# Optimization experiments

Measured on AMD Instinct MI355X. Metric: run time of the kernel, lower is better.

The kernel has to match this reference:

```python
import jax, jax.numpy as jnp
import numpy as np
from jax import lax

HIDDEN_MAX_ABS = 1000.0

def _run_layer(x_seq, W_ih, b_ih, w_hh, w_uh, b_uh, h0):
    # x_seq: [T,B,I]; W_ih: [H,I]; w_hh,w_uh,b_ih: [H]; b_uh: scalar; h0: [H]
    w_hh = jnp.clip(w_hh, -HIDDEN_MAX_ABS, HIDDEN_MAX_ABS)  # check_bounds (min_abs=0 is falsy)
    B = x_seq.shape[1]
    Hn = w_hh.shape[0]
    # hoist input projection out of the recurrence
    pre = jnp.einsum('tbi,hi->tbh', x_seq, W_ih) + b_ih  # [T,B,H]
    init = (jnp.broadcast_to(h0, (B, Hn)),
            jnp.ones((B, Hn), x_seq.dtype),
            jnp.zeros((B, Hn), x_seq.dtype))
    def step(carry, pre_t):
        hx, up_prev, cum_prev = carry
        new_hx = jax.nn.relu(pre_t + w_hh * hx)
        tilde = jax.nn.sigmoid(new_hx * w_uh + b_uh)
        cum = cum_prev + jnp.minimum(up_prev, 1.0 - cum_prev)
        # straight-through round (BinaryLayer)
        g = cum + lax.stop_gradient(jnp.round(cum) - cum)
        new_h = g * new_hx + (1.0 - g) * hx
        new_up = g * tilde + (1.0 - g) * up_prev
        new_cum = (1.0 - g) * cum
        return (new_h, new_up, new_cum), (new_h, g)
    _, (outs, gates) = lax.scan(step, init, pre)
    return outs, gates  # each [T,B,H]


def setup_inputs() -> dict:
    key = jax.random.key(0)
    ks = jax.random.split(key, 5)
    T, B, I, H, L = 512, 64, 256, 512, 2
    x = jax.random.normal(ks[0], (T, B, I), dtype=jnp.float32)
    h0 = jax.random.normal(ks[1], (L, H), dtype=jnp.float32)
    W_ih0 = 0.01 * jax.random.normal(ks[2], (H, I), dtype=jnp.float32)
    W_ih1 = 0.01 * jax.random.normal(ks[3], (H, H), dtype=jnp.float32)
    b_ih = jnp.zeros((L, H), jnp.float32)
    w_hh = jnp.ones((L, H), jnp.float32)
    w_uh = jax.random.normal(ks[4], (L, H), dtype=jnp.float32) * float(np.sqrt(2.0 / (1 + H)))
    b_uh = jnp.zeros((L,), jnp.float32)
    return {"x": x, "h0": h0, "W_ih0": W_ih0, "W_ih1": W_ih1,
            "b_ih": b_ih, "w_hh": w_hh, "w_uh": w_uh, "b_uh": b_uh}


def reference(x, h0, W_ih0, W_ih1, b_ih, w_hh, w_uh, b_uh):
    o0, g0 = _run_layer(x, W_ih0, b_ih[0], w_hh[0], w_uh[0], b_uh[0], h0[0])
    o1, g1 = _run_layer(o0, W_ih1, b_ih[1], w_hh[1], w_uh[1], b_uh[1], h0[1])
    # torch stacks layer outputs then .squeeze(); with L=2 no dim is squeezed
    x_out = jnp.stack([o0, o1], 0)      # [L,T,B,H]
    gates = jnp.stack([g0, g1], 0)      # [L,T,B,H]
    return x_out, gates
```

## Files before the change

kernel.cpp:

```cpp
#include <hip/hip_runtime.h>
#include <math.h>

#define TT 512
#define BB 64
#define II 256
#define HH 512
#define BH (BB*HH)
#define TBH ((size_t)TT*BH)
#define MM (TT*BB)

typedef float f32x4 __attribute__((ext_vector_type(4)));
typedef _Float16 f16x8 __attribute__((ext_vector_type(8)));
typedef unsigned short u16;

__device__ __forceinline__ void gload16(const void* g, void* l) {
    __builtin_amdgcn_global_load_lds(
        (const __attribute__((address_space(1))) unsigned int*)g,
        (__attribute__((address_space(3))) unsigned int*)l, 16, 0, 0);
}

__global__ __launch_bounds__(256)
void pack_w2(const float* __restrict__ W0, const float* __restrict__ W1,
             _Float16* __restrict__ P0, _Float16* __restrict__ P1,
             int nf0, int nf1)
{
    const int i = blockIdx.x * 256 + threadIdx.x;
    const float* src; _Float16* dst;
    if (i < nf0) { src = W0 + (size_t)i * 8;  dst = P0 + (size_t)i * 8; }
    else         { const int j = i - nf0; if (j >= nf1) return;
                   src = W1 + (size_t)j * 8;  dst = P1 + (size_t)j * 8; }
    f16x8 h8;
#pragma unroll
    for (int j = 0; j < 8; ++j) h8[j] = (_Float16)src[j];
    *(f16x8*)dst = h8;
}

template<typename OutT>
__global__ __launch_bounds__(256, 4)
void gemm_f32a(const float* __restrict__ A, const _Float16* __restrict__ Bp,
               const float* __restrict__ bias, OutT* __restrict__ C,
               int M, int N, int K)
{
    const int K8 = K >> 3;
    __shared__ _Float16 As[128][40];

    const int tid  = threadIdx.x;
    const int lane = tid & 63;
    const int wid  = tid >> 6;
    const int wr   = wid >> 1, wc = wid & 1;

    const int nbn = N >> 7;
    const int nt  = (M >> 7) * nbn;
    const int per = nt >> 3;
    const int logical = (blockIdx.x & 7) * per + (blockIdx.x >> 3);
    const int bm = logical / nbn;
    const int bn = logical % nbn;
    const int row0 = bm * 128;
    const int col0 = bn * 128;

    const int s_row = tid >> 1;
    const int s_kh  = (tid & 1) * 16;
    const float* Ap = A + (size_t)(row0 + s_row) * K + s_kh;

    const int fr  = lane & 15;
    const int q   = lane >> 4;
    const int ko8 = q * 8;

    f32x4 acc[4][4];
#pragma unroll
    for (int m = 0; m < 4; ++m)
#pragma unroll
        for (int n = 0; n < 4; ++n)
#pragma unroll
            for (int r = 0; r < 4; ++r) acc[m][n][r] = 0.f;

    const _Float16* bbase[4];
#pragma unroll
    for (int n = 0; n < 4; ++n) {
        const int col = col0 + wc * 64 + n * 16 + fr;
        bbase[n] = Bp + ((size_t)col * K8 + q) * 8;
    }

    f32x4 a_ld[4];
#pragma unroll
    for (int qq = 0; qq < 4; ++qq) a_ld[qq] = *(const f32x4*)(Ap + qq * 4);

    const int nkt = K >> 5;
    for (int kt = 0; kt < nkt; ++kt) {
        __syncthreads();
#pragma unroll
        for (int half = 0; half < 2; ++half) {
            f16x8 h8;
#pragma unroll
            for (int j = 0; j < 8; ++j)
                h8[j] = (_Float16)a_ld[half * 2 + (j >> 2)][j & 3];
            *(f16x8*)&As[s_row][s_kh + half * 8] = h8;
        }
        __syncthreads();

        f16x8 bfr[4];
#pragma unroll
        for (int n = 0; n < 4; ++n)
            bfr[n] = *(const f16x8*)(bbase[n] + (size_t)kt * 32);

        if (kt + 1 < nkt) {
            const float* apn = Ap + (size_t)(kt + 1) * 32;
#pragma unroll
            for (int qq = 0; qq < 4; ++qq) a_ld[qq] = *(const f32x4*)(apn + qq * 4);
        }

#pragma unroll
        for (int m = 0; m < 4; ++m) {
            const int row = wr * 64 + m * 16 + fr;
            f16x8 af = *(const f16x8*)&As[row][ko8];
#pragma unroll
            for (int n = 0; n < 4; ++n)
                acc[m][n] = __builtin_amdgcn_mfma_f32_16x16x32_f16(af, bfr[n], acc[m][n], 0, 0, 0);
        }
    }

#pragma unroll
    for (int n = 0; n < 4; ++n) {
        const int gc = col0 + wc * 64 + n * 16 + fr;
        const float bj = bias[gc];
#pragma unroll
        for (int m = 0; m < 4; ++m) {
            const int gr0 = row0 + wr * 64 + m * 16 + q * 4;
#pragma unroll
            for (int r = 0; r < 4; ++r)
                C[(size_t)(gr0 + r) * N + gc] = (OutT)(acc[m][n][r] + bj);
        }
    }
}

template<typename OutT>
__global__ __launch_bounds__(256, 3)
void gemm_f16a(const _Float16* __restrict__ A, const _Float16* __restrict__ Bp,
               const float* __restrict__ bias, OutT* __restrict__ C,
               int M, int N, int K)
{
    const int K8 = K >> 3;
    __shared__ _Float16 As[128 * 32];

    const int tid  = threadIdx.x;
    const int lane = tid & 63;
    const int wid  = tid >> 6;
    const int wr   = wid >> 1, wc = wid & 1;

    const int nbn = N >> 7;
    const int nt  = (M >> 7) * nbn;
    const int per = nt >> 3;
    const int logical = (blockIdx.x & 7) * per + (blockIdx.x >> 3);
    const int bm = logical / nbn;
    const int bn = logical % nbn;
    const int row0 = bm * 128;
    const int col0 = bn * 128;

    const int a_row = lane >> 2;
    const int a_kk  = (lane & 3) * 8;

    const int fr  = lane & 15;
    const int q   = lane >> 4;
    const int ko8 = q * 8;

    f32x4 acc[4][4];
#pragma unroll
    for (int m = 0; m < 4; ++m)
#pragma unroll
        for (int n = 0; n < 4; ++n)
#pragma unroll
            for (int r = 0; r < 4; ++r) acc[m][n][r] = 0.f;

    const _Float16* bbase[4];
#pragma unroll
    for (int n = 0; n < 4; ++n) {
        const int col = col0 + wc * 64 + n * 16 + fr;
        bbase[n] = Bp + ((size_t)col * K8 + q) * 8;
    }

    f16x8 bfr[4], bnf[4];
#pragma unroll
    for (int n = 0; n < 4; ++n) bfr[n] = *(const f16x8*)(bbase[n]);

    const int nkt = K >> 5;
    for (int kt = 0; kt < nkt; ++kt) {
        const int k0 = kt * 32;
        __syncthreads();
#pragma unroll
        for (int i = 0; i < 2; ++i) {
            const int chunk = wid * 2 + i;
            const size_t ga = (size_t)(row0 + chunk * 16 + a_row) * K + k0 + a_kk;
            gload16(A + ga, (char*)&As[0] + chunk * 1024 + (lane & 3) * 16
                               + (size_t)(a_row) * 0);
        }
        __syncthreads();

        if (kt + 1 < nkt) {
#pragma unroll
            for (int n = 0; n < 4; ++n)
                bnf[n] = *(const f16x8*)(bbase[n] + (size_t)(kt + 1) * 32);
        }

#pragma unroll
        for (int m = 0; m < 4; ++m) {
            const int row = wr * 64 + m * 16 + fr;
            f16x8 af = *(const f16x8*)&As[row * 32 + ko8];
#pragma unroll
            for (int n = 0; n < 4; ++n)
                acc[m][n] = __builtin_amdgcn_mfma_f32_16x16x32_f16(af, bfr[n], acc[m][n], 0, 0, 0);
        }
#pragma unroll
        for (int n = 0; n < 4; ++n) bfr[n] = bnf[n];
    }

#pragma unroll
    for (int n = 0; n < 4; ++n) {
        const int gc = col0 + wc * 64 + n * 16 + fr;
        const float bj = bias[gc];
#pragma unroll
        for (int m = 0; m < 4; ++m) {
            const int gr0 = row0 + wr * 64 + m * 16 + q * 4;
#pragma unroll
            for (int r = 0; r < 4; ++r)
                C[(size_t)(gr0 + r) * N + gc] = (OutT)(acc[m][n][r] + bj);
        }
    }
}

template<typename PreT, bool EMITF16, bool NTX, bool NTG>
__global__ __launch_bounds__(64)
void skip_indrnn_rec(const PreT* __restrict__ pre, const float* __restrict__ h0,
                     const float* __restrict__ w_hh, const float* __restrict__ w_uh,
                     const float* __restrict__ b_uh, int layer,
                     float* __restrict__ xo, float* __restrict__ go,
                     _Float16* __restrict__ xo16)
{
    const int idx = blockIdx.x * 64 + threadIdx.x;
    const int h = idx & (HH - 1);

    float whh = w_hh[layer * HH + h];
    whh = fminf(fmaxf(whh, -1000.f), 1000.f);
    const float wuh = w_uh[layer * HH + h];
    const float buh = b_uh[layer];

    float hx  = h0[layer * HH + h];
    float up  = 1.f;
    float cum = 0.f;

    const int SB = 16;
    const int NB = TT / SB;
    float cur[SB], nx1[SB], nx2[SB];
#pragma unroll
    for (int j = 0; j < SB; ++j) cur[j] = (float)pre[(size_t)j * BH + idx];
#pragma unroll
    for (int j = 0; j < SB; ++j) nx1[j] = (float)pre[(size_t)(SB + j) * BH + idx];

    for (int tb = 0; tb < NB; ++tb) {
        if (tb + 2 < NB) {
#pragma unroll
            for (int j = 0; j < SB; ++j)
                nx2[j] = (float)pre[(size_t)((tb + 2) * SB + j) * BH + idx];
        }
#pragma unroll
        for (int j = 0; j < SB; ++j) {
            const int t = tb * SB + j;
            const float nhx   = fmaxf(fmaf(whh, hx, cur[j]), 0.f);
            const float z     = fmaf(nhx, wuh, buh);
            const float tilde = 1.f / (1.f + __expf(-z));
            const float c     = cum + fminf(up, 1.f - cum);
            const float g     = rintf(c);
            const float nh    = (g > 0.5f) ? nhx   : hx;
            const float nup   = (g > 0.5f) ? tilde : up;
            const float ncum  = (g > 0.5f) ? 0.f   : c;
            if (NTX) __builtin_nontemporal_store(nh, &xo[(size_t)t * BH + idx]);
            else     xo[(size_t)t * BH + idx] = nh;
            if (NTG) __builtin_nontemporal_store(g, &go[(size_t)t * BH + idx]);
            else     go[(size_t)t * BH + idx] = g;
            if (EMITF16) {
                const _Float16 hv = (_Float16)nh;
                u16 bits; __builtin_memcpy(&bits, &hv, 2);
                __builtin_nontemporal_store(bits, (u16*)&xo16[(size_t)t * BH + idx]);
            }
            hx = nh; up = nup; cum = ncum;
        }
#pragma unroll
        for (int j = 0; j < SB; ++j) { cur[j] = nx1[j]; nx1[j] = nx2[j]; }
    }
}

extern "C" void kernel_launch(void* const* d_in, const int* in_sizes, int n_in,
                              void* d_out, int out_size, void* d_ws, size_t ws_size,
                              hipStream_t stream) {
    const float* x    = (const float*)d_in[0];
    const float* h0   = (const float*)d_in[1];
    const float* W0   = (const float*)d_in[2];
    const float* W1   = (const float*)d_in[3];
    const float* b_ih = (const float*)d_in[4];
    const float* w_hh = (const float*)d_in[5];
    const float* w_uh = (const float*)d_in[6];
    const float* b_uh = (const float*)d_in[7];

    float* out = (float*)d_out;
    float* X0 = out;
    float* X1 = out + TBH;
    float* G0 = out + 2 * TBH;
    float* G1 = out + 3 * TBH;

    const int nf0 = HH * II / 8;
    const int nf1 = HH * HH / 8;

    if (ws_size >= (size_t)100 * 1024 * 1024) {
        char* ws = (char*)d_ws;
        _Float16* P0    = (_Float16*)ws;
        _Float16* P1    = (_Float16*)(ws + (size_t)256 * 1024);
        _Float16* pre0  = (_Float16*)(ws + (size_t)1 * 1024 * 1024);
        _Float16* pre1  = (_Float16*)(ws + (size_t)33 * 1024 * 1024);
        _Float16* xo0h  = (_Float16*)(ws + (size_t)65 * 1024 * 1024);

        pack_w2<<<(nf0 + nf1 + 255) / 256, 256, 0, stream>>>(W0, W1, P0, P1, nf0, nf1);

        gemm_f32a<_Float16><<<1024, 256, 0, stream>>>(x, P0, b_ih, pre0, MM, HH, II);
        skip_indrnn_rec<_Float16, true, false, true><<<BH / 64, 64, 0, stream>>>(
            pre0, h0, w_hh, w_uh, b_uh, 0, X0, G0, xo0h);
        gemm_f16a<_Float16><<<1024, 256, 0, stream>>>(xo0h, P1, b_ih + HH, pre1, MM, HH, HH);
        skip_indrnn_rec<_Float16, false, true, true><<<BH / 64, 64, 0, stream>>>(
            pre1, h0, w_hh, w_uh, b_uh, 1, X1, G1, nullptr);
    } else {
        _Float16* P0 = (_Float16*)X1;
        _Float16* P1 = P0 + (size_t)nf0 * 8;
        float* pre = G1;

        pack_w2<<<(nf0 + nf1 + 255) / 256, 256, 0, stream>>>(W0, W1, P0, P1, nf0, nf1);

        gemm_f32a<float><<<1024, 256, 0, stream>>>(x, P0, b_ih, pre, MM, HH, II);
        skip_indrnn_rec<float, false, false, true><<<BH / 64, 64, 0, stream>>>(
            pre, h0, w_hh, w_uh, b_uh, 0, X0, G0, nullptr);
        gemm_f32a<float><<<1024, 256, 0, stream>>>(X0, P1, b_ih + HH, pre, MM, HH, HH);
        skip_indrnn_rec<float, false, true, true><<<BH / 64, 64, 0, stream>>>(
            pre, h0, w_hh, w_uh, b_uh, 1, X1, G1, nullptr);
    }
}
```

Baseline: 209.4 us.

## Stage GEMM A-tile through registers, deepen recurrence prefetch, adjust store hints

The f16 GEMM now loads A tiles into registers and writes them to a padded LDS array instead of using direct global-to-LDS loads. It drops the B double-buffer and raises occupancy to 4 blocks per CU. The recurrence kernel prefetches three time blocks ahead instead of two. Layer-0 fp32 outputs use nontemporal stores while the f16 copy is now a plain store so it can stay in cache for the next GEMM. These changes raise register pressure and leave B loads less hidden, in return for better latency hiding elsewhere.

```diff
diff --git a/kernel.cpp b/kernel.cpp
--- a/kernel.cpp
+++ b/kernel.cpp
@@ -12,12 +12,6 @@
 typedef float f32x4 __attribute__((ext_vector_type(4)));
 typedef _Float16 f16x8 __attribute__((ext_vector_type(8)));
 typedef unsigned short u16;
-
-__device__ __forceinline__ void gload16(const void* g, void* l) {
-    __builtin_amdgcn_global_load_lds(
-        (const __attribute__((address_space(1))) unsigned int*)g,
-        (__attribute__((address_space(3))) unsigned int*)l, 16, 0, 0);
-}
 
 __global__ __launch_bounds__(256)
 void pack_w2(const float* __restrict__ W0, const float* __restrict__ W1,
@@ -134,13 +128,13 @@
 }
 
 template<typename OutT>
-__global__ __launch_bounds__(256, 3)
-void gemm_f16a(const _Float16* __restrict__ A, const _Float16* __restrict__ Bp,
-               const float* __restrict__ bias, OutT* __restrict__ C,
-               int M, int N, int K)
+__global__ __launch_bounds__(256, 4)
+void gemm_f16a_reg(const _Float16* __restrict__ A, const _Float16* __restrict__ Bp,
+                   const float* __restrict__ bias, OutT* __restrict__ C,
+                   int M, int N, int K)
 {
     const int K8 = K >> 3;
-    __shared__ _Float16 As[128 * 32];
+    __shared__ _Float16 As[128][40];
 
     const int tid  = threadIdx.x;
     const int lane = tid & 63;
@@ -156,8 +150,9 @@
     const int row0 = bm * 128;
     const int col0 = bn * 128;
 
-    const int a_row = lane >> 2;
-    const int a_kk  = (lane & 3) * 8;
+    const int s_row = tid >> 1;
+    const int s_kh  = (tid & 1) * 16;
+    const _Float16* Ap = A + (size_t)(row0 + s_row) * K + s_kh;
 
     const int fr  = lane & 15;
     const int q   = lane >> 4;
@@ -178,39 +173,37 @@
         bbase[n] = Bp + ((size_t)col * K8 + q) * 8;
     }
 
-    f16x8 bfr[4], bnf[4];
-#pragma unroll
-    for (int n = 0; n < 4; ++n) bfr[n] = *(const f16x8*)(bbase[n]);
+    f16x8 a_ld[2];
+#pragma unroll
+    for (int hh = 0; hh < 2; ++hh) a_ld[hh] = *(const f16x8*)(Ap + hh * 8);
 
     const int nkt = K >> 5;
     for (int kt = 0; kt < nkt; ++kt) {
-        const int k0 = kt * 32;
         __syncthreads();
 #pragma unroll
-        for (int i = 0; i < 2; ++i) {
-            const int chunk = wid * 2 + i;
-            const size_t ga = (size_t)(row0 + chunk * 16 + a_row) * K + k0 + a_kk;
-            gload16(A + ga, (char*)&As[0] + chunk * 1024 + (lane & 3) * 16
-                               + (size_t)(a_row) * 0);
-        }
+        for (int hh = 0; hh < 2; ++hh)
+            *(f16x8*)&As[s_row][s_kh + hh * 8] = a_ld[hh];
         __syncthreads();
 
+        f16x8 bfr[4];
+#pragma unroll
+        for (int n = 0; n < 4; ++n)
+            bfr[n] = *(const f16x8*)(bbase[n] + (size_t)kt * 32);
+
         if (kt + 1 < nkt) {
-#pragma unroll
-            for (int n = 0; n < 4; ++n)
-                bnf[n] = *(const f16x8*)(bbase[n] + (size_t)(kt + 1) * 32);
+            const _Float16* apn = Ap + (size_t)(kt + 1) * 32;
+#pragma unroll
+            for (int hh = 0; hh < 2; ++hh) a_ld[hh] = *(const f16x8*)(apn + hh * 8);
         }
 
 #pragma unroll
         for (int m = 0; m < 4; ++m) {
             const int row = wr * 64 + m * 16 + fr;
-            f16x8 af = *(const f16x8*)&As[row * 32 + ko8];
+            f16x8 af = *(const f16x8*)&As[row][ko8];
 #pragma unroll
             for (int n = 0; n < 4; ++n)
                 acc[m][n] = __builtin_amdgcn_mfma_f32_16x16x32_f16(af, bfr[n], acc[m][n], 0, 0, 0);
         }
-#pragma unroll
-        for (int n = 0; n < 4; ++n) bfr[n] = bnf[n];
     }
 
 #pragma unroll
@@ -249,17 +242,19 @@
 
     const int SB = 16;
     const int NB = TT / SB;
-    float cur[SB], nx1[SB], nx2[SB];
+    float cur[SB], nx1[SB], nx2[SB], nx3[SB];
 #pragma unroll
     for (int j = 0; j < SB; ++j) cur[j] = (float)pre[(size_t)j * BH + idx];
 #pragma unroll
     for (int j = 0; j < SB; ++j) nx1[j] = (float)pre[(size_t)(SB + j) * BH + idx];
+#pragma unroll
+    for (int j = 0; j < SB; ++j) nx2[j] = (float)pre[(size_t)(2 * SB + j) * BH + idx];
 
     for (int tb = 0; tb < NB; ++tb) {
-        if (tb + 2 < NB) {
+        if (tb + 3 < NB) {
 #pragma unroll
             for (int j = 0; j < SB; ++j)
-                nx2[j] = (float)pre[(size_t)((tb + 2) * SB + j) * BH + idx];
+                nx3[j] = (float)pre[(size_t)((tb + 3) * SB + j) * BH + idx];
         }
 #pragma unroll
         for (int j = 0; j < SB; ++j) {
@@ -276,15 +271,12 @@
             else     xo[(size_t)t * BH + idx] = nh;
             if (NTG) __builtin_nontemporal_store(g, &go[(size_t)t * BH + idx]);
             else     go[(size_t)t * BH + idx] = g;
-            if (EMITF16) {
-                const _Float16 hv = (_Float16)nh;
-                u16 bits; __builtin_memcpy(&bits, &hv, 2);
-                __builtin_nontemporal_store(bits, (u16*)&xo16[(size_t)t * BH + idx]);
-            }
+            if (EMITF16)
+                xo16[(size_t)t * BH + idx] = (_Float16)nh;
             hx = nh; up = nup; cum = ncum;
         }
 #pragma unroll
-        for (int j = 0; j < SB; ++j) { cur[j] = nx1[j]; nx1[j] = nx2[j]; }
+        for (int j = 0; j < SB; ++j) { cur[j] = nx1[j]; nx1[j] = nx2[j]; nx2[j] = nx3[j]; }
     }
 }
 
@@ -311,18 +303,18 @@
 
     if (ws_size >= (size_t)100 * 1024 * 1024) {
         char* ws = (char*)d_ws;
-        _Float16* P0    = (_Float16*)ws;
-        _Float16* P1    = (_Float16*)(ws + (size_t)256 * 1024);
-        _Float16* pre0  = (_Float16*)(ws + (size_t)1 * 1024 * 1024);
-        _Float16* pre1  = (_Float16*)(ws + (size_t)33 * 1024 * 1024);
-        _Float16* xo0h  = (_Float16*)(ws + (size_t)65 * 1024 * 1024);
+        _Float16* P0   = (_Float16*)ws;
+        _Float16* P1   = (_Float16*)(ws + (size_t)256 * 1024);
+        _Float16* pre0 = (_Float16*)(ws + (size_t)1  * 1024 * 1024);
+        _Float16* pre1 = (_Float16*)(ws + (size_t)33 * 1024 * 1024);
+        _Float16* xo0h = (_Float16*)(ws + (size_t)65 * 1024 * 1024);
 
         pack_w2<<<(nf0 + nf1 + 255) / 256, 256, 0, stream>>>(W0, W1, P0, P1, nf0, nf1);
 
         gemm_f32a<_Float16><<<1024, 256, 0, stream>>>(x, P0, b_ih, pre0, MM, HH, II);
-        skip_indrnn_rec<_Float16, true, false, true><<<BH / 64, 64, 0, stream>>>(
+        skip_indrnn_rec<_Float16, true, true, true><<<BH / 64, 64, 0, stream>>>(
             pre0, h0, w_hh, w_uh, b_uh, 0, X0, G0, xo0h);
-        gemm_f16a<_Float16><<<1024, 256, 0, stream>>>(xo0h, P1, b_ih + HH, pre1, MM, HH, HH);
+        gemm_f16a_reg<_Float16><<<1024, 256, 0, stream>>>(xo0h, P1, b_ih + HH, pre1, MM, HH, HH);
         skip_indrnn_rec<_Float16, false, true, true><<<BH / 64, 64, 0, stream>>>(
             pre1, h0, w_hh, w_uh, b_uh, 1, X1, G1, nullptr);
     } else {
```

After: 208.7 us. About the same (-0.3%).
